# Kernel optimization log

Hardware: AMD Instinct MI355X
Metric: run time of the kernel (lower is better)

The kernel has to match this reference:

```python
import jax, jax.numpy as jnp
import numpy as np

B, T, OBS, S, OUT, H = 128, 2048, 128, 128, 64, 64
SCALE = 0.05  # keep the linear recurrence numerically stable over T steps


def setup_inputs() -> dict:
    key = jax.random.key(0)
    ks = jax.random.split(key, 8)
    return {
        "obs": jax.random.normal(ks[0], (B, T, OBS), dtype=jnp.float32),
        "x0": jnp.zeros((B, S), dtype=jnp.float32),
        "A_T": SCALE * jax.random.normal(ks[1], (S, S), dtype=jnp.float32),
        "By_T": SCALE * jax.random.normal(ks[2], (OBS, S), dtype=jnp.float32),
        "Cu_T": SCALE * jax.random.normal(ks[3], (S, OUT), dtype=jnp.float32),
        "Duy_T": SCALE * jax.random.normal(ks[4], (OBS, OUT), dtype=jnp.float32),
        "log_stds": jnp.full((OUT,), -1.6094379124341003, dtype=jnp.float32),
        "W0": SCALE * jax.random.normal(ks[5], (H, OBS), dtype=jnp.float32),
        "b0": jnp.zeros((H,), dtype=jnp.float32),
        "W1": SCALE * jax.random.normal(ks[6], (H, H), dtype=jnp.float32),
        "b1": jnp.zeros((H,), dtype=jnp.float32),
        "W2": SCALE * jax.random.normal(ks[7], (1, H), dtype=jnp.float32),
        "b2": jnp.zeros((1,), dtype=jnp.float32),
        "dt": jnp.float32(0.01),
    }


def reference(obs, x0, A_T, By_T, Cu_T, Duy_T, log_stds, W0, b0, W1, b1, W2, b2, dt):
    def xdot(x, y):
        return x @ A_T + y @ By_T

    def step(x, y):
        # control output at current state, then RK4 integration of x' = A x + B y
        u = x @ Cu_T + y @ Duy_T                      # [B, OUT]
        k1 = xdot(x, y)
        k2 = xdot(x + dt * k1 / 2, y)
        k3 = xdot(x + dt * k2 / 2, y)
        k4 = xdot(x + dt * k3, y)
        x_next = x + dt / 6 * (k1 + 2 * k2 + 2 * k3 + k4)
        return x_next, u

    obs_t = jnp.swapaxes(obs, 0, 1)                   # [T, B, OBS]
    x_final, actions_t = jax.lax.scan(step, x0, obs_t)
    actions = jnp.swapaxes(actions_t, 0, 1)           # [B, T, OUT]

    logs = jnp.broadcast_to(log_stds, (actions.shape[0], actions.shape[1], log_stds.shape[0]))
    outputs = jnp.concatenate([actions, logs], axis=2)  # [B, T, 2*OUT]

    # value MLP: Linear -> tanh -> Linear -> tanh -> Linear
    h = jnp.tanh(obs @ W0.T + b0)
    h = jnp.tanh(h @ W1.T + b1)
    cur_value = (h @ W2.T + b2).reshape(-1)           # [B*T]

    return outputs, cur_value, x_final
```

## Files before the change

kernel.cpp:

```cpp
#include <hip/hip_runtime.h>
#include <hip/hip_bf16.h>

#define B_    128
#define T_    2048
#define OBS_  128
#define S_    128
#define OUT_  64
#define H_    64
#define NR    (B_*T_)
#define K_CH  32
#define C_CH  64
#define VOFF  (NR*2*OUT_)
#define XFOFF (VOFF + NR)

typedef __attribute__((ext_vector_type(8))) short short8v;
typedef __attribute__((ext_vector_type(4))) float f32x4;

__device__ __forceinline__ unsigned short f2bf_hw(float f){
  __hip_bfloat16 h = __float2bfloat16(f);
  union { __hip_bfloat16 hh; unsigned short u; } cv; cv.hh = h; return cv.u;
}
__device__ __forceinline__ unsigned int pk2(float a, float b){
  __hip_bfloat162 h = __float22bfloat162_rn(make_float2(a, b));
  union { __hip_bfloat162 h2; unsigned int u; } cv; cv.h2 = h; return cv.u;
}
__device__ __forceinline__ float bf2f(unsigned short h){
  return __uint_as_float(((unsigned int)h) << 16);
}
__device__ __forceinline__ float fast_tanh(float x){
  float z = __builtin_exp2f(x * 2.88539008f);
  return 1.f - 2.f * __builtin_amdgcn_rcpf(z + 1.f);
}

__global__ __launch_bounds__(256) void k_mm(const float* __restrict__ A,
                                            const float* __restrict__ B,
                                            float* __restrict__ C, int ldc){
  int e = blockIdx.x * 256 + threadIdx.x;
  int r = e >> 7, c = e & 127;
  float acc = 0.f;
  #pragma unroll 4
  for (int k = 0; k < 128; ++k) acc += A[r*128 + k] * B[k*128 + c];
  C[r*ldc + c] = acc;
}

__global__ __launch_bounds__(256) void k_mm2(const float* __restrict__ A_T,
                                             const float* __restrict__ A2,
                                             float* __restrict__ A3,
                                             float* __restrict__ A4){
  int e = blockIdx.x * 256 + threadIdx.x;
  int r = e >> 7, c = e & 127;
  float a3 = 0.f, a4 = 0.f;
  #pragma unroll 4
  for (int k = 0; k < 128; ++k){
    float l = A2[r*128 + k];
    a3 += l * A_T[k*128 + c];
    a4 += l * A2[k*128 + c];
  }
  A3[e] = a3; A4[e] = a4;
}

__global__ __launch_bounds__(256) void k_build(const float* __restrict__ A_T,
                                               const float* __restrict__ A2,
                                               const float* __restrict__ A3,
                                               const float* __restrict__ A4,
                                               const float* __restrict__ Cu_T,
                                               const float* __restrict__ Duy_T,
                                               const float* __restrict__ dtp,
                                               float* __restrict__ M,
                                               unsigned short* __restrict__ Mmibf,
                                               float* __restrict__ P, float* __restrict__ Wcat,
                                               unsigned short* __restrict__ cubf){
  float dt = *dtp;
  float d2 = dt*dt*0.5f;
  float d3 = d2*dt*(1.f/3.f);
  float d4 = d3*dt*0.25f;
  int e = blockIdx.x * 256 + threadIdx.x;
  int r = e >> 7, c = e & 127;
  float eye = (r == c) ? 1.f : 0.f;
  float mi = dt*A_T[e] + d2*A2[e] + d3*A3[e] + d4*A4[e];
  M[e] = eye + mi;
  Mmibf[e] = f2bf_hw(mi);
  P[e] = dt*eye + d2*A_T[e] + d3*A2[e] + d4*A3[e];
  if (e < 128*64){
    int k = e >> 6, o = e & 63;
    Wcat[k*192 + 128 + o] = Duy_T[e];
    cubf[e] = f2bf_hw(Cu_T[e]);
  }
}

__global__ __launch_bounds__(256) void k_gm2(const float* __restrict__ By_T,
                                             const float* __restrict__ Pp,
                                             const float* __restrict__ Mm,
                                             float* __restrict__ Wcat,
                                             float* __restrict__ sq1){
  int e = blockIdx.x * 256 + threadIdx.x;
  int r = e >> 7, c = e & 127;
  float ga = 0.f, m2 = 0.f;
  #pragma unroll 4
  for (int k = 0; k < 128; ++k){
    ga += By_T[r*128 + k] * Pp[k*128 + c];
    m2 += Mm[r*128 + k] * Mm[k*128 + c];
  }
  Wcat[r*192 + c] = ga;
  sq1[e] = m2;
}

__global__ __launch_bounds__(256) void k_m4cvt(const float* __restrict__ sq1,
                                               const float* __restrict__ Wcat,
                                               const float* __restrict__ W0,
                                               const float* __restrict__ W1,
                                               float* __restrict__ sq2,
                                               unsigned short* __restrict__ Wbf,
                                               unsigned short* __restrict__ W0bf,
                                               unsigned short* __restrict__ W1bf){
  int e = blockIdx.x * 256 + threadIdx.x;
  int r = e >> 7, c = e & 127;
  float m4 = 0.f;
  #pragma unroll 4
  for (int k = 0; k < 128; ++k) m4 += sq1[r*128 + k] * sq1[k*128 + c];
  sq2[e] = m4;
  for (int i = e; i < 24576; i += 16384) Wbf[i] = f2bf_hw(Wcat[i]);
  if (e < 8192) W0bf[e] = f2bf_hw(W0[e]);
  if (e < 4096) W1bf[e] = f2bf_hw(W1[e]);
}

__global__ __launch_bounds__(256) void k_fused(const float* __restrict__ obs,
                                               const unsigned short* __restrict__ Wbf,
                                               const unsigned short* __restrict__ W0bf,
                                               const unsigned short* __restrict__ W1bf,
                                               const float* __restrict__ W2,
                                               const float* __restrict__ b0g,
                                               const float* __restrict__ b1g,
                                               const float* __restrict__ b2g,
                                               const float* __restrict__ ls,
                                               unsigned short* __restrict__ cuy,
                                               float* __restrict__ out){
  __shared__ __align__(16) unsigned short ylds[64*136];
  __shared__ __align__(16) unsigned short ct[16*200];
  __shared__ __align__(16) unsigned short h0l[64*80];
  __shared__ float pl[64][4];
  int tid = threadIdx.x;
  int lane = tid & 63, w = tid >> 6;
  size_t row0 = (size_t)blockIdx.x * 128;
  int colbase = w * 48;
  int colh    = w * 16;
  int lr = lane & 15;
  int lk = (lane >> 4) * 8;

  short8v bfrag[3][4];
  #pragma unroll
  for (int cf = 0; cf < 3; ++cf)
    #pragma unroll
    for (int kk = 0; kk < 4; ++kk){
      short8v b;
      #pragma unroll
      for (int j = 0; j < 8; ++j)
        b[j] = (short)Wbf[(size_t)(kk*32 + lk + j)*192 + (colbase + cf*16 + lr)];
      bfrag[cf][kk] = b;
    }
  short8v bw0[4];
  #pragma unroll
  for (int kk = 0; kk < 4; ++kk)
    bw0[kk] = *(const short8v*)&W0bf[(size_t)(colh + lr)*128 + kk*32 + lk];
  short8v bw1[2];
  #pragma unroll
  for (int kk = 0; kk < 2; ++kk)
    bw1[kk] = *(const short8v*)&W1bf[(size_t)(colh + lr)*64 + kk*32 + lk];
  float b0v = b0g[colh + lr];
  float b1v = b1g[colh + lr];
  float w2v = W2[colh + lr];

  for (int h = 0; h < 2; ++h){
    {
      int base = tid * 32;
      int r = base >> 7, c0 = base & 127;
      const float* grow = obs + (row0 + h*64 + r) * 128;
      #pragma unroll
      for (int it = 0; it < 4; ++it){
        float4 a0 = *(const float4*)&grow[c0 + it*8];
        float4 a1 = *(const float4*)&grow[c0 + it*8 + 4];
        uint4 pv;
        pv.x = pk2(a0.x, a0.y); pv.y = pk2(a0.z, a0.w);
        pv.z = pk2(a1.x, a1.y); pv.w = pk2(a1.z, a1.w);
        *(uint4*)&ylds[r*136 + c0 + it*8] = pv;
      }
    }
    __syncthreads();
    for (int rfh = 0; rfh < 4; ++rfh){
      f32x4 acc0 = {0.f,0.f,0.f,0.f}, acc1 = {0.f,0.f,0.f,0.f}, acc2 = {0.f,0.f,0.f,0.f};
      f32x4 acch = {0.f,0.f,0.f,0.f};
      #pragma unroll
      for (int kk = 0; kk < 4; ++kk){
        short8v af = *(const short8v*)&ylds[(rfh*16 + lr)*136 + kk*32 + lk];
        acc0 = __builtin_amdgcn_mfma_f32_16x16x32_bf16(af, bfrag[0][kk], acc0, 0, 0, 0);
        acc1 = __builtin_amdgcn_mfma_f32_16x16x32_bf16(af, bfrag[1][kk], acc1, 0, 0, 0);
        acc2 = __builtin_amdgcn_mfma_f32_16x16x32_bf16(af, bfrag[2][kk], acc2, 0, 0, 0);
        acch = __builtin_amdgcn_mfma_f32_16x16x32_bf16(af, bw0[kk],     acch, 0, 0, 0);
      }
      int hrow = rfh*16 + (lane >> 4)*4;
      int crow = (lane >> 4)*4;
      #pragma unroll
      for (int j = 0; j < 4; ++j){
        ct[(crow + j)*200 + colbase      + lr] = f2bf_hw(acc0[j]);
        ct[(crow + j)*200 + colbase + 16 + lr] = f2bf_hw(acc1[j]);
        ct[(crow + j)*200 + colbase + 32 + lr] = f2bf_hw(acc2[j]);
        h0l[(hrow + j)*80 + colh + lr]         = f2bf_hw(fast_tanh(acch[j] + b0v));
      }
      __syncthreads();
      for (int li = tid; li < 16*24; li += 256){
        int r = li / 24, seg = li % 24;
        *(uint4*)&cuy[(row0 + h*64 + rfh*16 + r)*192 + seg*8] = *(const uint4*)&ct[r*200 + seg*8];
      }
      __syncthreads();
    }
    for (int rf = 0; rf < 4; ++rf){
      f32x4 acc = {b1v, b1v, b1v, b1v};
      #pragma unroll
      for (int kk = 0; kk < 2; ++kk){
        short8v af = *(const short8v*)&h0l[(rf*16 + lr)*80 + kk*32 + lk];
        acc = __builtin_amdgcn_mfma_f32_16x16x32_bf16(af, bw1[kk], acc, 0, 0, 0);
      }
      float4 vpart;
      #pragma unroll
      for (int j = 0; j < 4; ++j) (&vpart.x)[j] = fast_tanh(acc[j]) * w2v;
      #pragma unroll
      for (int m = 1; m < 16; m <<= 1){
        vpart.x += __shfl_xor(vpart.x, m);
        vpart.y += __shfl_xor(vpart.y, m);
        vpart.z += __shfl_xor(vpart.z, m);
        vpart.w += __shfl_xor(vpart.w, m);
      }
      if (lr == 0){
        int hrow = rf*16 + (lane >> 4)*4;
        #pragma unroll
        for (int j = 0; j < 4; ++j) pl[hrow + j][w] = (&vpart.x)[j];
      }
    }
    __syncthreads();
    if (tid < 64)
      out[(size_t)VOFF + row0 + h*64 + tid] = pl[tid][0] + pl[tid][1] + pl[tid][2] + pl[tid][3] + b2g[0];
    __syncthreads();
  }

  for (int li = tid; li < 128*16; li += 256){
    int r = li >> 4, c4 = li & 15;
    float4 lv = *(const float4*)&ls[c4*4];
    *(float4*)&out[(row0 + r)*128 + 64 + c4*4] = lv;
  }
}

__global__ __launch_bounds__(256) void k_phase1(const unsigned short* __restrict__ cuy,
                                                const unsigned short* __restrict__ Mmibf,
                                                float* __restrict__ Dd){
  __shared__ __align__(16) unsigned short xwA[16*136];
  __shared__ __align__(16) unsigned short xwB[16*136];
  int tid = threadIdx.x;
  int lane = tid & 63, w = tid >> 6;
  int lr = lane & 15, lg = lane >> 4;
  int pr = blockIdx.x >> 3, bi = blockIdx.x & 7;
  int b0 = bi*16;
  int ciA = 2*pr, ciB = 2*pr + 1;
  int t0A = ciA*K_CH, t0B = ciB*K_CH;
  int colbase = w*32;

  short8v bm[2][4];
  #pragma unroll
  for (int ctt = 0; ctt < 2; ++ctt)
    #pragma unroll
    for (int kk = 0; kk < 4; ++kk){
      short8v b;
      #pragma unroll
      for (int j = 0; j < 8; ++j)
        b[j] = (short)Mmibf[(size_t)(kk*32 + lg*8 + j)*128 + colbase + ctt*16 + lr];
      bm[ctt][kk] = b;
    }

  f32x4 accA[2], accB[2];
  #pragma unroll
  for (int ctt = 0; ctt < 2; ++ctt)
    #pragma unroll
    for (int j = 0; j < 4; ++j){
      size_t rb = (size_t)(b0 + lg*4 + j)*T_;
      accA[ctt][j] = bf2f(cuy[(rb + t0A)*192 + colbase + ctt*16 + lr]);
      accB[ctt][j] = bf2f(cuy[(rb + t0B)*192 + colbase + ctt*16 + lr]);
    }

  for (int s = 1; s < K_CH; ++s){
    unsigned short cnA[2][4], cnB[2][4];
    #pragma unroll
    for (int ctt = 0; ctt < 2; ++ctt)
      #pragma unroll
      for (int j = 0; j < 4; ++j){
        size_t rb = (size_t)(b0 + lg*4 + j)*T_;
        cnA[ctt][j] = cuy[(rb + t0A + s)*192 + colbase + ctt*16 + lr];
        cnB[ctt][j] = cuy[(rb + t0B + s)*192 + colbase + ctt*16 + lr];
      }
    #pragma unroll
    for (int ctt = 0; ctt < 2; ++ctt)
      #pragma unroll
      for (int j = 0; j < 4; ++j){
        xwA[(lg*4 + j)*136 + colbase + ctt*16 + lr] = f2bf_hw(accA[ctt][j]);
        xwB[(lg*4 + j)*136 + colbase + ctt*16 + lr] = f2bf_hw(accB[ctt][j]);
      }
    __syncthreads();
    short8v afA[4], afB[4];
    #pragma unroll
    for (int kk = 0; kk < 4; ++kk){
      afA[kk] = *(const short8v*)&xwA[lr*136 + kk*32 + lg*8];
      afB[kk] = *(const short8v*)&xwB[lr*136 + kk*32 + lg*8];
    }
    __syncthreads();
    #pragma unroll
    for (int ctt = 0; ctt < 2; ++ctt)
      #pragma unroll
      for (int kk = 0; kk < 4; ++kk)
        accA[ctt] = __builtin_amdgcn_mfma_f32_16x16x32_bf16(afA[kk], bm[ctt][kk], accA[ctt], 0, 0, 0);
    #pragma unroll
    for (int ctt = 0; ctt < 2; ++ctt)
      #pragma unroll
      for (int kk = 0; kk < 4; ++kk)
        accB[ctt] = __builtin_amdgcn_mfma_f32_16x16x32_bf16(afB[kk], bm[ctt][kk], accB[ctt], 0, 0, 0);
    #pragma unroll
    for (int ctt = 0; ctt < 2; ++ctt)
      #pragma unroll
      for (int j = 0; j < 4; ++j){
        accA[ctt][j] += bf2f(cnA[ctt][j]);
        accB[ctt][j] += bf2f(cnB[ctt][j]);
      }
  }
  #pragma unroll
  for (int ctt = 0; ctt < 2; ++ctt)
    #pragma unroll
    for (int j = 0; j < 4; ++j){
      Dd[(size_t)ciA*16384 + (size_t)(b0 + lg*4 + j)*128 + colbase + ctt*16 + lr] = accA[ctt][j];
      Dd[(size_t)ciB*16384 + (size_t)(b0 + lg*4 + j)*128 + colbase + ctt*16 + lr] = accB[ctt][j];
    }
}

__global__ __launch_bounds__(256) void k_combine(const float* __restrict__ Mk,
                                                 const float* __restrict__ Dd,
                                                 const float* __restrict__ x0,
                                                 float* __restrict__ XS,
                                                 float* __restrict__ xfin){
  __shared__ float xl[128];
  __shared__ float pl[256];
  int tid = threadIdx.x;
  int b = blockIdx.x;
  int c = tid & 127, h = tid >> 7;
  float mreg[64];
  #pragma unroll
  for (int j = 0; j < 64; ++j) mreg[j] = Mk[(64*h + j)*128 + c];
  if (tid < 128) xl[tid] = x0[(size_t)b*128 + tid];
  __syncthreads();
  for (int i = 0; i < C_CH; ++i){
    if (tid < 128) XS[(size_t)i*16384 + (size_t)b*128 + tid] = xl[tid];
    float part = 0.f;
    #pragma unroll
    for (int jj = 0; jj < 64; jj += 4){
      float4 xv = *(const float4*)&xl[64*h + jj];
      part += xv.x*mreg[jj] + xv.y*mreg[jj+1] + xv.z*mreg[jj+2] + xv.w*mreg[jj+3];
    }
    pl[tid] = part;
    __syncthreads();
    if (tid < 128)
      xl[tid] = pl[tid] + pl[tid + 128] + Dd[(size_t)i*16384 + (size_t)b*128 + tid];
    __syncthreads();
  }
  if (tid < 128) xfin[(size_t)b*128 + tid] = xl[tid];
}

__global__ __launch_bounds__(256) void k_phase3(const unsigned short* __restrict__ cuy,
                                                const unsigned short* __restrict__ Mmibf,
                                                const unsigned short* __restrict__ cubf,
                                                const float* __restrict__ XS,
                                                float* __restrict__ out){
  __shared__ __align__(16) unsigned short xwA[16*136];
  __shared__ __align__(16) unsigned short xwB[16*136];
  int tid = threadIdx.x;
  int lane = tid & 63, w = tid >> 6;
  int lr = lane & 15, lg = lane >> 4;
  int pr = blockIdx.x >> 3, bi = blockIdx.x & 7;
  int b0 = bi*16;
  int ciA = 2*pr, ciB = 2*pr + 1;
  int t0A = ciA*K_CH, t0B = ciB*K_CH;
  int colbase = w*32;
  int ucolbase = w*16;

  short8v bm[2][4];
  #pragma unroll
  for (int ctt = 0; ctt < 2; ++ctt)
    #pragma unroll
    for (int kk = 0; kk < 4; ++kk){
      short8v b;
      #pragma unroll
      for (int j = 0; j < 8; ++j)
        b[j] = (short)Mmibf[(size_t)(kk*32 + lg*8 + j)*128 + colbase + ctt*16 + lr];
      bm[ctt][kk] = b;
    }
  short8v bc[4];
  #pragma unroll
  for (int kk = 0; kk < 4; ++kk){
    short8v b;
    #pragma unroll
    for (int j = 0; j < 8; ++j)
      b[j] = (short)cubf[(size_t)(kk*32 + lg*8 + j)*64 + ucolbase + lr];
    bc[kk] = b;
  }

  f32x4 accA[2], accB[2];
  #pragma unroll
  for (int ctt = 0; ctt < 2; ++ctt)
    #pragma unroll
    for (int j = 0; j < 4; ++j){
      size_t xb = (size_t)(b0 + lg*4 + j)*128 + colbase + ctt*16 + lr;
      accA[ctt][j] = XS[(size_t)ciA*16384 + xb];
      accB[ctt][j] = XS[(size_t)ciB*16384 + xb];
    }

  for (int s = 0; s < K_CH; ++s){
    f32x4 auA, auB;
    #pragma unroll
    for (int j = 0; j < 4; ++j){
      size_t rb = (size_t)(b0 + lg*4 + j)*T_;
      auA[j] = bf2f(cuy[(rb + t0A + s)*192 + 128 + ucolbase + lr]);
      auB[j] = bf2f(cuy[(rb + t0B + s)*192 + 128 + ucolbase + lr]);
    }
    unsigned short cnA[2][4], cnB[2][4];
    if (s + 1 < K_CH){
      #pragma unroll
      for (int ctt = 0; ctt < 2; ++ctt)
        #pragma unroll
        for (int j = 0; j < 4; ++j){
          size_t rb = (size_t)(b0 + lg*4 + j)*T_;
          cnA[ctt][j] = cuy[(rb + t0A + s)*192 + colbase + ctt*16 + lr];
          cnB[ctt][j] = cuy[(rb + t0B + s)*192 + colbase + ctt*16 + lr];
        }
    }
    #pragma unroll
    for (int ctt = 0; ctt < 2; ++ctt)
      #pragma unroll
      for (int j = 0; j < 4; ++j){
        xwA[(lg*4 + j)*136 + colbase + ctt*16 + lr] = f2bf_hw(accA[ctt][j]);
        xwB[(lg*4 + j)*136 + colbase + ctt*16 + lr] = f2bf_hw(accB[ctt][j]);
      }
    __syncthreads();
    short8v afA[4], afB[4];
    #pragma unroll
    for (int kk = 0; kk < 4; ++kk){
      afA[kk] = *(const short8v*)&xwA[lr*136 + kk*32 + lg*8];
      afB[kk] = *(const short8v*)&xwB[lr*136 + kk*32 + lg*8];
    }
    __syncthreads();
    #pragma unroll
    for (int kk = 0; kk < 4; ++kk){
      auA = __builtin_amdgcn_mfma_f32_16x16x32_bf16(afA[kk], bc[kk], auA, 0, 0, 0);
      auB = __builtin_amdgcn_mfma_f32_16x16x32_bf16(afB[kk], bc[kk], auB, 0, 0, 0);
    }
    #pragma unroll
    for (int j = 0; j < 4; ++j){
      size_t rb = (size_t)(b0 + lg*4 + j)*T_;
      out[(rb + t0A + s)*128 + ucolbase + lr] = auA[j];
      out[(rb + t0B + s)*128 + ucolbase + lr] = auB[j];
    }
    if (s + 1 < K_CH){
      #pragma unroll
      for (int ctt = 0; ctt < 2; ++ctt)
        #pragma unroll
        for (int kk = 0; kk < 4; ++kk)
          accA[ctt] = __builtin_amdgcn_mfma_f32_16x16x32_bf16(afA[kk], bm[ctt][kk], accA[ctt], 0, 0, 0);
      #pragma unroll
      for (int ctt = 0; ctt < 2; ++ctt)
        #pragma unroll
        for (int kk = 0; kk < 4; ++kk)
          accB[ctt] = __builtin_amdgcn_mfma_f32_16x16x32_bf16(afB[kk], bm[ctt][kk], accB[ctt], 0, 0, 0);
      #pragma unroll
      for (int ctt = 0; ctt < 2; ++ctt)
        #pragma unroll
        for (int j = 0; j < 4; ++j){
          accA[ctt][j] += bf2f(cnA[ctt][j]);
          accB[ctt][j] += bf2f(cnB[ctt][j]);
        }
    }
  }
}

extern "C" void kernel_launch(void* const* d_in, const int* in_sizes, int n_in,
                              void* d_out, int out_size, void* d_ws, size_t ws_size,
                              hipStream_t stream){
  const float* obs  = (const float*)d_in[0];
  const float* x0   = (const float*)d_in[1];
  const float* A_T  = (const float*)d_in[2];
  const float* By_T = (const float*)d_in[3];
  const float* Cu_T = (const float*)d_in[4];
  const float* Duy_T= (const float*)d_in[5];
  const float* ls   = (const float*)d_in[6];
  const float* W0   = (const float*)d_in[7];
  const float* b0   = (const float*)d_in[8];
  const float* W1   = (const float*)d_in[9];
  const float* b1   = (const float*)d_in[10];
  const float* W2   = (const float*)d_in[11];
  const float* b2   = (const float*)d_in[12];
  const float* dt   = (const float*)d_in[13];
  float* out = (float*)d_out;

  char* ws = (char*)d_ws;
  unsigned short* cuy = (unsigned short*)(ws + 0);
  float* A2     = (float*)(ws + 100663296);
  float* A3     = (float*)(ws + 100728832);
  float* A4     = (float*)(ws + 100794368);
  float* Mm     = (float*)(ws + 100859904);
  float* Pp     = (float*)(ws + 100925440);
  float* Mk     = (float*)(ws + 100990976);
  float* sq1    = (float*)(ws + 101056512);
  float* sq2    = (float*)(ws + 101122048);
  unsigned short* Mmibf = (unsigned short*)(ws + 101187584);
  float* Wcat   = (float*)(ws + 101255168);
  unsigned short* cubf  = (unsigned short*)(ws + 101353472);
  float* Dd     = (float*)(ws + 101387264);
  float* XS     = (float*)(ws + 105581568);
  unsigned short* Wbf  = (unsigned short*)Pp;
  unsigned short* W0bf = (unsigned short*)A3;
  unsigned short* W1bf = (unsigned short*)A4;

  k_mm   <<<64, 256, 0, stream>>>(A_T, A_T, A2, 128);
  k_mm2  <<<64, 256, 0, stream>>>(A_T, A2, A3, A4);
  k_build<<<64, 256, 0, stream>>>(A_T, A2, A3, A4, Cu_T, Duy_T, dt, Mm, Mmibf, Pp, Wcat, cubf);
  k_gm2  <<<64, 256, 0, stream>>>(By_T, Pp, Mm, Wcat, sq1);
  k_m4cvt<<<64, 256, 0, stream>>>(sq1, Wcat, W0, W1, sq2, Wbf, W0bf, W1bf);
  k_mm   <<<64, 256, 0, stream>>>(sq2, sq2, sq1, 128);
  k_mm   <<<64, 256, 0, stream>>>(sq1, sq1, sq2, 128);
  k_mm   <<<64, 256, 0, stream>>>(sq2, sq2, Mk, 128);

  k_fused<<<NR/128, 256, 0, stream>>>(obs, Wbf, W0bf, W1bf, W2, b0, b1, b2, ls, cuy, out);
  k_phase1<<<(C_CH/2)*8, 256, 0, stream>>>(cuy, Mmibf, Dd);
  k_combine<<<B_, 256, 0, stream>>>(Mk, Dd, x0, XS, out + XFOFF);
  k_phase3<<<(C_CH/2)*8, 256, 0, stream>>>(cuy, Mmibf, cubf, XS, out);
}
```

Measured before the change: 280.8 us.

## Double-buffer staging tile, prefetch Dd in combine, move log_std writes to phase3

In k_fused, the staging tile for cuy is double-buffered across row fragments so one barrier per fragment is dropped. k_combine prefetches the next chunk's Dd value before the reduction, taking the global load off the serial recurrence's critical path. The log_std half of the output is now written in k_phase3 next to the action columns instead of in a separate loop at the end of k_fused. Moving those writes makes phase3's stores touch full 128-float rows, but each is a scalar store interleaved with the MFMA loop.

```diff
diff --git a/kernel.cpp b/kernel.cpp
--- a/kernel.cpp
+++ b/kernel.cpp
@@ -132,11 +132,10 @@
                                                const float* __restrict__ b0g,
                                                const float* __restrict__ b1g,
                                                const float* __restrict__ b2g,
-                                               const float* __restrict__ ls,
                                                unsigned short* __restrict__ cuy,
                                                float* __restrict__ out){
   __shared__ __align__(16) unsigned short ylds[64*136];
-  __shared__ __align__(16) unsigned short ct[16*200];
+  __shared__ __align__(16) unsigned short ct[2][16*200];
   __shared__ __align__(16) unsigned short h0l[64*80];
   __shared__ float pl[64][4];
   int tid = threadIdx.x;
@@ -199,19 +198,19 @@
       }
       int hrow = rfh*16 + (lane >> 4)*4;
       int crow = (lane >> 4)*4;
+      unsigned short* ctb = ct[rfh & 1];
       #pragma unroll
       for (int j = 0; j < 4; ++j){
-        ct[(crow + j)*200 + colbase      + lr] = f2bf_hw(acc0[j]);
-        ct[(crow + j)*200 + colbase + 16 + lr] = f2bf_hw(acc1[j]);
-        ct[(crow + j)*200 + colbase + 32 + lr] = f2bf_hw(acc2[j]);
-        h0l[(hrow + j)*80 + colh + lr]         = f2bf_hw(fast_tanh(acch[j] + b0v));
+        ctb[(crow + j)*200 + colbase      + lr] = f2bf_hw(acc0[j]);
+        ctb[(crow + j)*200 + colbase + 16 + lr] = f2bf_hw(acc1[j]);
+        ctb[(crow + j)*200 + colbase + 32 + lr] = f2bf_hw(acc2[j]);
+        h0l[(hrow + j)*80 + colh + lr]          = f2bf_hw(fast_tanh(acch[j] + b0v));
       }
       __syncthreads();
       for (int li = tid; li < 16*24; li += 256){
         int r = li / 24, seg = li % 24;
-        *(uint4*)&cuy[(row0 + h*64 + rfh*16 + r)*192 + seg*8] = *(const uint4*)&ct[r*200 + seg*8];
-      }
-      __syncthreads();
+        *(uint4*)&cuy[(row0 + h*64 + rfh*16 + r)*192 + seg*8] = *(const uint4*)&ctb[r*200 + seg*8];
+      }
     }
     for (int rf = 0; rf < 4; ++rf){
       f32x4 acc = {b1v, b1v, b1v, b1v};
@@ -240,12 +239,6 @@
     if (tid < 64)
       out[(size_t)VOFF + row0 + h*64 + tid] = pl[tid][0] + pl[tid][1] + pl[tid][2] + pl[tid][3] + b2g[0];
     __syncthreads();
-  }
-
-  for (int li = tid; li < 128*16; li += 256){
-    int r = li >> 4, c4 = li & 15;
-    float4 lv = *(const float4*)&ls[c4*4];
-    *(float4*)&out[(row0 + r)*128 + 64 + c4*4] = lv;
   }
 }
 
@@ -351,9 +344,13 @@
   #pragma unroll
   for (int j = 0; j < 64; ++j) mreg[j] = Mk[(64*h + j)*128 + c];
   if (tid < 128) xl[tid] = x0[(size_t)b*128 + tid];
+  float dcur = (tid < 128) ? Dd[(size_t)b*128 + tid] : 0.f;
   __syncthreads();
   for (int i = 0; i < C_CH; ++i){
     if (tid < 128) XS[(size_t)i*16384 + (size_t)b*128 + tid] = xl[tid];
+    float dnext = 0.f;
+    if (i + 1 < C_CH && tid < 128)
+      dnext = Dd[(size_t)(i+1)*16384 + (size_t)b*128 + tid];
     float part = 0.f;
     #pragma unroll
     for (int jj = 0; jj < 64; jj += 4){
@@ -363,8 +360,9 @@
     pl[tid] = part;
     __syncthreads();
     if (tid < 128)
-      xl[tid] = pl[tid] + pl[tid + 128] + Dd[(size_t)i*16384 + (size_t)b*128 + tid];
-    __syncthreads();
+      xl[tid] = pl[tid] + pl[tid + 128] + dcur;
+    __syncthreads();
+    dcur = dnext;
   }
   if (tid < 128) xfin[(size_t)b*128 + tid] = xl[tid];
 }
@@ -373,6 +371,7 @@
                                                 const unsigned short* __restrict__ Mmibf,
                                                 const unsigned short* __restrict__ cubf,
                                                 const float* __restrict__ XS,
+                                                const float* __restrict__ ls,
                                                 float* __restrict__ out){
   __shared__ __align__(16) unsigned short xwA[16*136];
   __shared__ __align__(16) unsigned short xwB[16*136];
@@ -385,6 +384,7 @@
   int t0A = ciA*K_CH, t0B = ciB*K_CH;
   int colbase = w*32;
   int ucolbase = w*16;
+  float lsv = ls[ucolbase + lr];
 
   short8v bm[2][4];
   #pragma unroll
@@ -459,8 +459,10 @@
     #pragma unroll
     for (int j = 0; j < 4; ++j){
       size_t rb = (size_t)(b0 + lg*4 + j)*T_;
-      out[(rb + t0A + s)*128 + ucolbase + lr] = auA[j];
-      out[(rb + t0B + s)*128 + ucolbase + lr] = auB[j];
+      out[(rb + t0A + s)*128 + ucolbase + lr]       = auA[j];
+      out[(rb + t0A + s)*128 + 64 + ucolbase + lr]  = lsv;
+      out[(rb + t0B + s)*128 + ucolbase + lr]       = auB[j];
+      out[(rb + t0B + s)*128 + 64 + ucolbase + lr]  = lsv;
     }
     if (s + 1 < K_CH){
       #pragma unroll
@@ -531,8 +533,8 @@
   k_mm   <<<64, 256, 0, stream>>>(sq1, sq1, sq2, 128);
   k_mm   <<<64, 256, 0, stream>>>(sq2, sq2, Mk, 128);
 
-  k_fused<<<NR/128, 256, 0, stream>>>(obs, Wbf, W0bf, W1bf, W2, b0, b1, b2, ls, cuy, out);
+  k_fused<<<NR/128, 256, 0, stream>>>(obs, Wbf, W0bf, W1bf, W2, b0, b1, b2, cuy, out);
   k_phase1<<<(C_CH/2)*8, 256, 0, stream>>>(cuy, Mmibf, Dd);
   k_combine<<<B_, 256, 0, stream>>>(Mk, Dd, x0, XS, out + XFOFF);
-  k_phase3<<<(C_CH/2)*8, 256, 0, stream>>>(cuy, Mmibf, cubf, XS, out);
-}
+  k_phase3<<<(C_CH/2)*8, 256, 0, stream>>>(cuy, Mmibf, cubf, XS, ls, out);
+}
```

Result: no change. 276.6 us (-1.5%).
